# Kernel tuning notes

Measured on AMD Instinct MI355X. Metric: run time of the kernel, lower is better.

Reference implementation:

```python
import jax, jax.numpy as jnp
import numpy as np

B, L, E, DA, R = 256, 2048, 64, 64, 32

def setup_inputs() -> dict:
    key = jax.random.key(0)
    k1, k2, k3, k4 = jax.random.split(key, 4)
    x = jax.random.normal(k1, (B, L, E), dtype=jnp.float32)
    mask = (jax.random.uniform(k2, (B, L)) > 0.2).astype(jnp.float32)
    # glorot-uniform-like init for the small attention weights
    lim1 = np.sqrt(6.0 / (DA + E)).astype(np.float32)
    lim2 = np.sqrt(6.0 / (R + DA)).astype(np.float32)
    W1 = jax.random.uniform(k3, (DA, E), minval=-lim1, maxval=lim1, dtype=jnp.float32)
    W2 = jax.random.uniform(k4, (R, DA), minval=-lim2, maxval=lim2, dtype=jnp.float32)
    return {"x": x, "mask": mask, "W1": W1, "W2": W2}

def reference(x, mask, W1, W2):
    # x: (B,L,E), mask: (B,L), W1: (DA,E), W2: (R,DA)
    xm = x * mask[:, :, None]                       # masked inputs (B,L,E)
    H = jnp.tanh(jnp.einsum('de,ble->bdl', W1, xm))  # (B,DA,L)
    Q = jnp.einsum('rd,bdl->brl', W2, H)             # (B,R,L)
    A = jnp.exp(Q) * mask[:, None, :]                # masked exp scores (B,R,L)
    A = A / jnp.sum(A, axis=2, keepdims=True)        # normalize over L
    # dropout is identity at inference
    return jnp.einsum('brl,ble->bre', A, xm)         # (B,R,E)
```

## Files before the change

kernel.cpp:

```cpp
#include <hip/hip_runtime.h>
#include <hip/hip_bf16.h>


#define B_  256
#define L_  2048
#define E_  64
#define DA_ 64
#define R_  32
#define CH_ 8
#define NS_ 4
#define TL_ 64

typedef __attribute__((ext_vector_type(8))) short bf16x8;
typedef __attribute__((ext_vector_type(4))) float f32x4;

#define HS_P 36
#define XT_P 36
#define AS_P 36
#define HS_W (64 * HS_P)
#define XT_W (64 * XT_P)
#define AS_W (32 * AS_P)

__device__ __forceinline__ unsigned pk(float a, float b) {
    __hip_bfloat162 h = __float22bfloat162_rn(float2{a, b});
    union { __hip_bfloat162 h2; unsigned u; } cv; cv.h2 = h;
    return cv.u;
}
__device__ __forceinline__ float bflo(unsigned u) { return __uint_as_float(u << 16); }
__device__ __forceinline__ float bfhi(unsigned u) { return __uint_as_float(u & 0xFFFF0000u); }
__device__ __forceinline__ float fast_tanh(float v) {
    float e = __builtin_amdgcn_exp2f(v * 2.885390082f);
    float r = __builtin_amdgcn_rcpf(e + 1.0f);
    return fmaf(-2.0f, r, 1.0f);
}
__device__ __forceinline__ float fast_exp(float v) {
    return __builtin_amdgcn_exp2f(v * 1.442695041f);
}

__launch_bounds__(256, 5)
__global__ void selfbi_main(const float* __restrict__ x,
                            const float* __restrict__ mask,
                            const float* __restrict__ W1,
                            const float* __restrict__ W2,
                            float* __restrict__ accp,
                            float* __restrict__ ssump) {
    __shared__ __align__(16) unsigned smem[HS_W + XT_W + AS_W + 128];
    unsigned* hsw = smem;
    unsigned* xtw = smem + HS_W;
    unsigned* asw = xtw + XT_W;
    float*    ssl = (float*)(asw + AS_W);

    const int b    = blockIdx.x;
    const int c    = blockIdx.y;
    const int tid  = threadIdx.x;
    const int w    = tid >> 6;
    const int lane = tid & 63;
    const int g    = lane >> 4;
    const int ml   = lane & 15;

    bf16x8 w1f[4][2], w2f[2][2];
    #pragma unroll
    for (int mt = 0; mt < 4; ++mt)
        #pragma unroll
        for (int kb = 0; kb < 2; ++kb) {
            const float* p = W1 + (16 * mt + ml) * E_ + 32 * kb + 8 * g;
            float4 a = *(const float4*)p, bb = *(const float4*)(p + 4);
            union { bf16x8 s; unsigned u[4]; } cv;
            cv.u[0] = pk(a.x, a.y); cv.u[1] = pk(a.z, a.w);
            cv.u[2] = pk(bb.x, bb.y); cv.u[3] = pk(bb.z, bb.w);
            w1f[mt][kb] = cv.s;
        }
    #pragma unroll
    for (int nt = 0; nt < 2; ++nt)
        #pragma unroll
        for (int kb = 0; kb < 2; ++kb) {
            const float* p = W2 + (16 * nt + ml) * DA_ + 32 * kb + 8 * g;
            float4 a = *(const float4*)p, bb = *(const float4*)(p + 4);
            union { bf16x8 s; unsigned u[4]; } cv;
            cv.u[0] = pk(a.x, a.y); cv.u[1] = pk(a.z, a.w);
            cv.u[2] = pk(bb.x, bb.y); cv.u[3] = pk(bb.z, bb.w);
            w2f[nt][kb] = cv.s;
        }

    f32x4 c3[2] = {f32x4{0,0,0,0}, f32x4{0,0,0,0}};
    float sswav0 = 0.0f, sswav1 = 0.0f;

    const int trow = 16 * w + ml;
    const int thalf = trow >> 1, tbyte = trow & 1;

    for (int s = 0; s < NS_; ++s) {
        if (s) __syncthreads();

        const int    l0    = c * (NS_ * TL_) + s * TL_;
        const size_t xbase = ((size_t)b * L_ + l0) * E_;

        const float* xr = x + xbase + (size_t)trow * E_;
        float4 gx[2][2];
        gx[0][0] = *(const float4*)(xr + 8 * g);
        gx[0][1] = *(const float4*)(xr + 8 * g + 4);
        gx[1][0] = *(const float4*)(xr + 32 + 8 * g);
        gx[1][1] = *(const float4*)(xr + 32 + 8 * g + 4);
        float4 mk = *(const float4*)(mask + b * L_ + l0 + 16 * w + 4 * g);

        bf16x8 xf[2];
        union { bf16x8 s; unsigned u[4]; } xc[2];
        #pragma unroll
        for (int kb = 0; kb < 2; ++kb) {
            xc[kb].u[0] = pk(gx[kb][0].x, gx[kb][0].y);
            xc[kb].u[1] = pk(gx[kb][0].z, gx[kb][0].w);
            xc[kb].u[2] = pk(gx[kb][1].x, gx[kb][1].y);
            xc[kb].u[3] = pk(gx[kb][1].z, gx[kb][1].w);
            xf[kb] = xc[kb].s;
        }

        #pragma unroll
        for (int kb = 0; kb < 2; ++kb)
            #pragma unroll
            for (int i = 0; i < 4; ++i) {
                const int e0 = 32 * kb + 8 * g + 2 * i;
                const int wd = thalf ^ (8 * g);
                ((unsigned short*)&xtw[e0 * XT_P + wd])[tbyte] =
                    (unsigned short)(xc[kb].u[i] & 0xFFFF);
                ((unsigned short*)&xtw[(e0 + 1) * XT_P + wd])[tbyte] =
                    (unsigned short)(xc[kb].u[i] >> 16);
            }

        f32x4 c1[4] = {f32x4{0,0,0,0}, f32x4{0,0,0,0}, f32x4{0,0,0,0}, f32x4{0,0,0,0}};
        #pragma unroll
        for (int kb = 0; kb < 2; ++kb)
            #pragma unroll
            for (int mt = 0; mt < 4; ++mt)
                c1[mt] = __builtin_amdgcn_mfma_f32_16x16x32_bf16(
                    w1f[mt][kb], xf[kb], c1[mt], 0, 0, 0);

        #pragma unroll
        for (int mt = 0; mt < 4; ++mt) {
            float h0 = fast_tanh(c1[mt][0]);
            float h1 = fast_tanh(c1[mt][1]);
            float h2 = fast_tanh(c1[mt][2]);
            float h3 = fast_tanh(c1[mt][3]);
            uint2 u; u.x = pk(h0, h1); u.y = pk(h2, h3);
            *(uint2*)&hsw[trow * HS_P + 8 * mt + 2 * g] = u;
        }

        f32x4 c2[2] = {f32x4{0,0,0,0}, f32x4{0,0,0,0}};
        #pragma unroll
        for (int kb = 0; kb < 2; ++kb) {
            bf16x8 af = *(bf16x8*)&hsw[trow * HS_P + 16 * kb + 4 * g];
            #pragma unroll
            for (int nt = 0; nt < 2; ++nt)
                c2[nt] = __builtin_amdgcn_mfma_f32_16x16x32_bf16(
                    af, w2f[nt][kb], c2[nt], 0, 0, 0);
        }

        float part0, part1;
        {
            const int tw = 8 * w + 2 * g;
            float a0 = fast_exp(c2[0][0]) * mk.x;
            float a1 = fast_exp(c2[0][1]) * mk.y;
            float a2 = fast_exp(c2[0][2]) * mk.z;
            float a3 = fast_exp(c2[0][3]) * mk.w;
            uint2 u; u.x = pk(a0, a1); u.y = pk(a2, a3);
            *(uint2*)&asw[ml * AS_P + tw] = u;
            part0 = bflo(u.x) + bfhi(u.x) + bflo(u.y) + bfhi(u.y);
            a0 = fast_exp(c2[1][0]) * mk.x;
            a1 = fast_exp(c2[1][1]) * mk.y;
            a2 = fast_exp(c2[1][2]) * mk.z;
            a3 = fast_exp(c2[1][3]) * mk.w;
            u.x = pk(a0, a1); u.y = pk(a2, a3);
            *(uint2*)&asw[(16 + ml) * AS_P + tw] = u;
            part1 = bflo(u.x) + bfhi(u.x) + bflo(u.y) + bfhi(u.y);
        }
        part0 += __shfl_xor(part0, 16); part0 += __shfl_xor(part0, 32);
        part1 += __shfl_xor(part1, 16); part1 += __shfl_xor(part1, 32);
        sswav0 += part0; sswav1 += part1;

        __syncthreads();

        {
            const int erow = 16 * w + ml;
            const int esw  = 8 * ((erow >> 3) & 3);
            #pragma unroll
            for (int kb = 0; kb < 2; ++kb) {
                bf16x8 bf = *(bf16x8*)&xtw[erow * XT_P + ((16 * kb + 4 * g) ^ esw)];
                #pragma unroll
                for (int mt = 0; mt < 2; ++mt) {
                    bf16x8 af = *(bf16x8*)&asw[(16 * mt + ml) * AS_P + 16 * kb + 4 * g];
                    c3[mt] = __builtin_amdgcn_mfma_f32_16x16x32_bf16(af, bf, c3[mt], 0, 0, 0);
                }
            }
        }
    }

    const size_t obase = (size_t)(b * CH_ + c) * (R_ * E_);
    const int e = 16 * w + ml;
    #pragma unroll
    for (int mt = 0; mt < 2; ++mt)
        #pragma unroll
        for (int reg = 0; reg < 4; ++reg) {
            const int r = 16 * mt + 4 * g + reg;
            accp[obase + r * E_ + e] = c3[mt][reg];
        }
    if (g == 0) {
        ssl[w * 32 + ml]      = sswav0;
        ssl[w * 32 + 16 + ml] = sswav1;
    }
    __syncthreads();
    if (tid < 32)
        ssump[(b * CH_ + c) * R_ + tid] =
            ssl[tid] + ssl[32 + tid] + ssl[64 + tid] + ssl[96 + tid];
}

__launch_bounds__(256, 4)
__global__ void selfbi_reduce(const float* __restrict__ accp,
                              const float* __restrict__ ssump,
                              float* __restrict__ out) {
    const int of = blockIdx.x * 256 + threadIdx.x;
    const int b  = of >> 11;
    const int o  = of & 2047;
    const int r  = o >> 6;
    float num = 0.f, den = 0.f;
    #pragma unroll
    for (int cc = 0; cc < CH_; ++cc) {
        num += accp[((size_t)(b * CH_ + cc)) * (R_ * E_) + o];
        den += ssump[(b * CH_ + cc) * R_ + r];
    }
    out[of] = num / den;
}

extern "C" void kernel_launch(void* const* d_in, const int* in_sizes, int n_in,
                              void* d_out, int out_size, void* d_ws, size_t ws_size,
                              hipStream_t stream) {
    const float* x    = (const float*)d_in[0];
    const float* mask = (const float*)d_in[1];
    const float* W1   = (const float*)d_in[2];
    const float* W2   = (const float*)d_in[3];
    float* out        = (float*)d_out;

    float* accp  = (float*)d_ws;
    float* ssump = accp + (size_t)B_ * CH_ * R_ * E_;

    selfbi_main<<<dim3(B_, CH_), dim3(256), 0, stream>>>(x, mask, W1, W2, accp, ssump);
    selfbi_reduce<<<dim3((B_ * R_ * E_) / 256), dim3(256), 0, stream>>>(accp, ssump, out);
}
```

Measured before the change: 248.3 us.

## Prefetch next tile of x and mask into registers with double-buffered LDS

```diff
diff --git a/kernel.cpp b/kernel.cpp
--- a/kernel.cpp
+++ b/kernel.cpp
@@ -37,18 +37,18 @@
     return __builtin_amdgcn_exp2f(v * 1.442695041f);
 }
 
-__launch_bounds__(256, 5)
+__launch_bounds__(256, 4)
 __global__ void selfbi_main(const float* __restrict__ x,
                             const float* __restrict__ mask,
                             const float* __restrict__ W1,
                             const float* __restrict__ W2,
                             float* __restrict__ accp,
                             float* __restrict__ ssump) {
-    __shared__ __align__(16) unsigned smem[HS_W + XT_W + AS_W + 128];
-    unsigned* hsw = smem;
-    unsigned* xtw = smem + HS_W;
-    unsigned* asw = xtw + XT_W;
-    float*    ssl = (float*)(asw + AS_W);
+    __shared__ __align__(16) unsigned smem[HS_W + 2 * XT_W + 2 * AS_W + 128];
+    unsigned* hsw  = smem;
+    unsigned* xtw0 = smem + HS_W;
+    unsigned* asw0 = xtw0 + 2 * XT_W;
+    float*    ssl  = (float*)(asw0 + 2 * AS_W);
 
     const int b    = blockIdx.x;
     const int c    = blockIdx.y;
@@ -85,22 +85,24 @@
     f32x4 c3[2] = {f32x4{0,0,0,0}, f32x4{0,0,0,0}};
     float sswav0 = 0.0f, sswav1 = 0.0f;
 
-    const int trow = 16 * w + ml;
+    const int trow  = 16 * w + ml;
     const int thalf = trow >> 1, tbyte = trow & 1;
+    const size_t cbase = ((size_t)b * L_ + c * (NS_ * TL_)) * E_;
+    const int    mbase = b * L_ + c * (NS_ * TL_);
+
+    float4 gx[2][2], mk;
+    {
+        const float* xr = x + cbase + (size_t)trow * E_ + 8 * g;
+        gx[0][0] = *(const float4*)xr;
+        gx[0][1] = *(const float4*)(xr + 4);
+        gx[1][0] = *(const float4*)(xr + 32);
+        gx[1][1] = *(const float4*)(xr + 36);
+        mk = *(const float4*)(mask + mbase + 16 * w + 4 * g);
+    }
 
     for (int s = 0; s < NS_; ++s) {
-        if (s) __syncthreads();
-
-        const int    l0    = c * (NS_ * TL_) + s * TL_;
-        const size_t xbase = ((size_t)b * L_ + l0) * E_;
-
-        const float* xr = x + xbase + (size_t)trow * E_;
-        float4 gx[2][2];
-        gx[0][0] = *(const float4*)(xr + 8 * g);
-        gx[0][1] = *(const float4*)(xr + 8 * g + 4);
-        gx[1][0] = *(const float4*)(xr + 32 + 8 * g);
-        gx[1][1] = *(const float4*)(xr + 32 + 8 * g + 4);
-        float4 mk = *(const float4*)(mask + b * L_ + l0 + 16 * w + 4 * g);
+        unsigned* xtw = xtw0 + (s & 1) * XT_W;
+        unsigned* asw = asw0 + (s & 1) * AS_W;
 
         bf16x8 xf[2];
         union { bf16x8 s; unsigned u[4]; } xc[2];
@@ -111,6 +113,16 @@
             xc[kb].u[2] = pk(gx[kb][1].x, gx[kb][1].y);
             xc[kb].u[3] = pk(gx[kb][1].z, gx[kb][1].w);
             xf[kb] = xc[kb].s;
+        }
+
+        float4 gxn[2][2], mkn;
+        if (s + 1 < NS_) {
+            const float* xr = x + cbase + (size_t)((s + 1) * TL_ + trow) * E_ + 8 * g;
+            gxn[0][0] = *(const float4*)xr;
+            gxn[0][1] = *(const float4*)(xr + 4);
+            gxn[1][0] = *(const float4*)(xr + 32);
+            gxn[1][1] = *(const float4*)(xr + 36);
+            mkn = *(const float4*)(mask + mbase + (s + 1) * TL_ + 16 * w + 4 * g);
         }
 
         #pragma unroll
@@ -190,6 +202,10 @@
                 }
             }
         }
+
+        gx[0][0] = gxn[0][0]; gx[0][1] = gxn[0][1];
+        gx[1][0] = gxn[1][0]; gx[1][1] = gxn[1][1];
+        mk = mkn;
     }
 
     const size_t obase = (size_t)(b * CH_ + c) * (R_ * E_);
```

Measured after the change: 207.7 us. 16.4% less time.
